# Optimization experiments

Measured on AMD Instinct MI355X. Metric: run time of the kernel, lower is better.

## Reference

```python
import jax, jax.numpy as jnp
import numpy as np
from collections import deque

SIGMA_LOW = 0.02  # TreeFilter2D(sigma=0.02); high-level trees use sigma=1 (low_tree=False)


def bilinear_resize(x, oh, ow):
    # torch F.interpolate(mode='bilinear', align_corners=False)
    B, C, H, W = x.shape
    sy, sx = H / oh, W / ow
    ys = jnp.maximum((jnp.arange(oh, dtype=jnp.float32) + 0.5) * sy - 0.5, 0.0)
    xs = jnp.maximum((jnp.arange(ow, dtype=jnp.float32) + 0.5) * sx - 0.5, 0.0)
    y0 = jnp.clip(jnp.floor(ys).astype(jnp.int32), 0, H - 1)
    x0 = jnp.clip(jnp.floor(xs).astype(jnp.int32), 0, W - 1)
    y1 = jnp.minimum(y0 + 1, H - 1)
    x1 = jnp.minimum(x0 + 1, W - 1)
    wy = (ys - y0).reshape(oh, 1)
    wx = (xs - x0).reshape(1, ow)
    top, bot = x[:, :, y0, :], x[:, :, y1, :]
    v00, v01 = top[:, :, :, x0], top[:, :, :, x1]
    v10, v11 = bot[:, :, :, x0], bot[:, :, :, x1]
    return ((1 - wy) * (1 - wx)) * v00 + ((1 - wy) * wx) * v01 + (wy * (1 - wx)) * v10 + (wy * wx) * v11


def nearest_resize(x, oh, ow):
    B, C, H, W = x.shape
    yi = jnp.minimum((jnp.arange(oh) * (H / oh)).astype(jnp.int32), H - 1)
    xi = jnp.minimum((jnp.arange(ow) * (W / ow)).astype(jnp.int32), W - 1)
    return x[:, :, yi, :][:, :, :, xi]


def _mst_adj(feat, h, w):
    # Kruskal MST on 4-connected grid; edge weight = norm2_distance of features.
    n = h * w
    idx = np.arange(n).reshape(h, w)
    eu = np.concatenate([idx[:, :-1].ravel(), idx[:-1, :].ravel()])
    ev = np.concatenate([idx[:, 1:].ravel(), idx[1:, :].ravel()])
    f = feat.reshape(feat.shape[0], -1).astype(np.float64)
    d = ((f[:, eu] - f[:, ev]) ** 2).sum(axis=0)
    order = np.argsort(d, kind='stable')
    pa = np.arange(n)

    def find(a):
        r = a
        while pa[r] != r:
            r = pa[r]
        while pa[a] != r:
            pa[a], a = r, pa[a]
        return r

    adj = [[] for _ in range(n)]
    cnt = 0
    for e in order:
        u, v = int(eu[e]), int(ev[e])
        ru, rv = find(u), find(v)
        if ru != rv:
            pa[ru] = rv
            adj[u].append(v)
            adj[v].append(u)
            cnt += 1
            if cnt == n - 1:
                break
    return adj


def build_forest(embed):
    # embed: np [B,C,h,w] -> global parent array (ids b*n+i) + per-BFS-level node lists
    B, C, h, w = embed.shape
    n = h * w
    parent = np.arange(B * n)
    level = np.zeros(B * n, dtype=np.int64)
    for b in range(B):
        adj = _mst_adj(embed[b], h, w)
        lv = np.full(n, -1, dtype=np.int64)
        lv[0] = 0
        q = deque([0])
        while q:
            u = q.popleft()
            for v in adj[u]:
                if lv[v] < 0:
                    lv[v] = lv[u] + 1
                    parent[b * n + v] = b * n + u
                    q.append(v)
        level[b * n:(b + 1) * n] = lv
    d = int(level.max())
    levels = [np.nonzero(level == l)[0] for l in range(1, d + 1)]
    return jnp.asarray(parent), levels


def tree_filter(feature, embed, parent, levels, sigma):
    # feature [B,C,n], embed [B,Ce,n]; normalized tree filtering:
    # y_i = sum_j prod(path-edge-weights) x_j / sum_j prod(path-edge-weights)
    B, C, n = feature.shape
    ones = jnp.ones((B, 1, n), feature.dtype)
    xg = jnp.moveaxis(jnp.concatenate([feature, ones], axis=1), 0, 1).reshape(C + 1, B * n)
    eg = jnp.moveaxis(embed, 0, 1).reshape(embed.shape[1], B * n)
    wgt = jnp.exp(-((eg - eg[:, parent]) ** 2).sum(axis=0) / sigma)  # [B*n]; root entries unused
    # upward (leaf->root) subtree aggregation
    A = xg
    for idx in reversed(levels):
        A = A.at[:, parent[idx]].add(wgt[idx] * A[:, idx])
    # downward (root->leaf) completion
    F = A
    for idx in levels:
        F = F.at[:, idx].set(A[:, idx] + wgt[idx] * (F[:, parent[idx]] - wgt[idx] * A[:, idx]))
    y = F[:C] / F[C]
    return jnp.moveaxis(y.reshape(C, B, n), 0, 1)  # [B,C,n]


def setup_inputs() -> dict:
    key = jax.random.key(0)
    ks = jax.random.split(key, 6)
    B, K, h, w = 8, 4, 48, 48
    C = 512
    preds = jax.random.normal(ks[0], (B, K, h, w), jnp.float32)
    low_feats = jax.random.uniform(ks[1], (B, 3, 192, 192), jnp.float32) * 0.1
    hf1 = jax.random.normal(ks[2], (B, C, 24, 24), jnp.float32) * 0.05
    hf2 = jax.random.normal(ks[3], (B, C, 12, 12), jnp.float32) * 0.05
    hf3 = jax.random.normal(ks[4], (B, C, 6, 6), jnp.float32) * 0.05
    rois = (jax.random.uniform(ks[5], (B, 192, 192)) > 0.5).astype(jnp.float32)
    weight = jnp.asarray(0.4, jnp.float32)
    return {"preds": preds, "low_feats": low_feats, "high_feats_1": hf1,
            "high_feats_2": hf2, "high_feats_3": hf3, "unlabeled_ROIs": rois,
            "weight": weight}


def reference(preds, low_feats, high_feats_1, high_feats_2, high_feats_3, unlabeled_ROIs, weight):
    B, K, h, w = preds.shape
    low = bilinear_resize(low_feats, h, w)                     # no_grad in original
    roi = nearest_resize(unlabeled_ROIs[:, None], h, w)        # [B,1,h,w]
    N = roi.sum()
    prob = jax.nn.softmax(preds, axis=1)
    probf = prob.reshape(B, K, -1)
    roif = roi.reshape(B, 1, -1)

    parent0, lv0 = build_forest(np.asarray(low))
    AS = tree_filter(probf, low.reshape(B, low.shape[1], -1), parent0, lv0, SIGMA_LOW)

    loss = jnp.zeros((), preds.dtype)
    for hf in (high_feats_1, high_feats_2, high_feats_3):
        hfi = bilinear_resize(hf, h, w)
        p, lv = build_forest(np.asarray(hfi))
        AS_k = tree_filter(AS, hfi.reshape(B, hfi.shape[1], -1), p, lv, 1.0)
        loss = loss + (roif * jnp.abs(probf - AS_k)).sum()
    loss = jnp.where(N > 0, loss / N, loss)
    return weight * loss
```

## Files before the change

### kernel.cpp

```cpp
#include <hip/hip_runtime.h>
#include <math.h>


#define HH 48
#define WW 48
#define NN (HH*WW)
#define EHH (HH*(WW-1))
#define EEE (2*EHH)
#define BB 8
#define KK 4
#define TPB 256
#define TPE 512
#define TPW 1024
#define TPF 512
#define NPL 5
#define NPN 5
#define LVE (2*(NN-1))
#define NIPT ((NN+TPW-1)/TPW)
#define SENTN 0xFFFFu
#define MAXT 12

__device__ __forceinline__ void edge_uv(int e,int& u,int& v){
  if(e<EHH){ int r=e/(WW-1); int c=e-r*(WW-1); u=r*WW+c; v=u+1; }
  else     { int t=e-EHH; u=t; v=t+WW; }
}

__device__ __forceinline__ void pick_src(int f, const float* lowf, const float* hf1,
                                         const float* hf2, const float* hf3,
                                         const float*& src, int& sh, int& C){
  if(f==0){src=lowf; sh=192; C=3;}
  else if(f==1){src=hf1; sh=24; C=512;}
  else if(f==2){src=hf2; sh=12; C=512;}
  else        {src=hf3; sh=6;  C=512;}
}

__global__ __launch_bounds__(TPE) void k_edges(
  const float* __restrict__ lowf, const float* __restrict__ hf1,
  const float* __restrict__ hf2, const float* __restrict__ hf3,
  const float* __restrict__ preds, float* __restrict__ probf,
  double* __restrict__ pd_low, double* __restrict__ pd_hf, int nchunk)
{
  __shared__ float up[4*NN+64];
  __shared__ int   y0t[48], y1t[48];
  __shared__ float wyt[48];
  const int tid=threadIdx.x;
  const int nEB=8+24*nchunk;

  if(blockIdx.x>=nEB){
    int t=(blockIdx.x-nEB)*TPE+tid;
    if(t<BB*NN){
      int b=t/NN, i=t-b*NN;
      const float* p=preds+(size_t)b*KK*NN+i;
      float x0=p[0],x1=p[NN],x2=p[2*NN],x3=p[3*NN];
      float mx=fmaxf(fmaxf(x0,x1),fmaxf(x2,x3));
      float e0=expf(x0-mx),e1=expf(x1-mx),e2=expf(x2-mx),e3=expf(x3-mx);
      float s=((e0+e1)+(e2+e3));
      float* q=probf+(size_t)b*KK*NN+i;
      q[0]=e0/s; q[NN]=e1/s; q[2*NN]=e2/s; q[3*NN]=e3/s;
    }
    return;
  }

  int pidx, chunk, hfidx=0;
  if(blockIdx.x<8){ pidx=blockIdx.x; chunk=0; }
  else { int t=blockIdx.x-8; hfidx=t/nchunk; chunk=t-hfidx*nchunk; pidx=8+hfidx; }
  const int f=pidx>>3, b=pidx&7;
  const float* src; int sh,C;
  pick_src(f,lowf,hf1,hf2,hf3,src,sh,C);
  const int shw=sh*sh;
  const float* srcb=src+(size_t)b*C*shw;
  const int cpc=(f==0)?3:(512/nchunk);
  const int c_begin=chunk*cpc;
  const int c_end=(c_begin+cpc<C)?(c_begin+cpc):C;

  if(tid<48){
    float sy=(float)sh/48.0f;
    float ys=fmaxf(((float)tid+0.5f)*sy-0.5f,0.0f);
    int y0=(int)ys; if(y0>sh-1) y0=sh-1;
    int y1=y0+1; if(y1>sh-1) y1=sh-1;
    y0t[tid]=y0; y1t[tid]=y1; wyt[tid]=ys-(float)y0;
  }

  double accH[NPN], accV[NPN];
  #pragma unroll
  for(int j=0;j<NPN;j++){ accH[j]=0.0; accV[j]=0.0; }

  for(int c0=c_begin;c0<c_end;c0+=4){
    const int nc=(c_end-c0<4)?(c_end-c0):4;
    __syncthreads();
    for(int i=tid;i<NN;i+=TPE){
      int r=i/WW, c=i-r*WW;
      int y0=y0t[r], y1=y1t[r]; float wy=wyt[r];
      int x0=y0t[c], x1=y1t[c]; float wx=wyt[c];
      float w00=(1.0f-wy)*(1.0f-wx), w01=(1.0f-wy)*wx;
      float w10=wy*(1.0f-wx),        w11=wy*wx;
      int o00=y0*sh+x0, o01=y0*sh+x1, o10=y1*sh+x0, o11=y1*sh+x1;
      const float* pl=srcb+(size_t)c0*shw;
      for(int cc=0;cc<nc;cc++){
        const float* p=pl+(size_t)cc*shw;
        up[cc*NN+i]=w00*p[o00]+w01*p[o01]+w10*p[o10]+w11*p[o11];
      }
    }
    __syncthreads();
    #pragma unroll
    for(int j=0;j<NPN;j++){
      int u=tid+j*TPE;
      if(u<NN){
        int r=u/WW, c=u-r*WW;
        bool hOK=(c<WW-1), vOK=(r<HH-1);
        for(int cc=0;cc<nc;cc++){
          const float* pu=up+cc*NN+u;
          float a=pu[0], b1=pu[1], c1=pu[WW];
          if(hOK){ double d=(double)a-(double)b1; accH[j]=fma(d,d,accH[j]); }
          if(vOK){ double d=(double)a-(double)c1; accV[j]=fma(d,d,accV[j]); }
        }
      }
    }
  }
  double* outp=(f==0)? pd_low+(size_t)pidx*EEE
                     : pd_hf+((size_t)hfidx*nchunk+chunk)*EEE;
  #pragma unroll
  for(int j=0;j<NPN;j++){
    int u=tid+j*TPE;
    if(u<NN){
      int r=u/WW, c=u-r*WW;
      if(c<WW-1) outp[r*(WW-1)+c]=accH[j];
      if(r<HH-1) outp[EHH+u]=accV[j];
    }
  }
}

__global__ __launch_bounds__(TPB) void k_redux(
  const double* __restrict__ pd_low, const double* __restrict__ pd_hf,
  int nchunk, double* __restrict__ dkeyG, int* __restrict__ cnt)
{
  int t=blockIdx.x*TPB+threadIdx.x;
  if(t==0) *cnt=0;
  if(t>=32*EEE) return;
  int pidx=t/EEE, e=t-pidx*EEE;
  double s;
  if(pidx<8) s=pd_low[(size_t)pidx*EEE+e];
  else {
    const double* p0=pd_hf+((size_t)(pidx-8)*nchunk)*EEE+e;
    s=0.0;
    for(int k=0;k<nchunk;k++) s+=p0[(size_t)k*EEE];
  }
  dkeyG[t]=s;
}

__global__ __launch_bounds__(TPW) void k_struct(
  const double* __restrict__ dkeyG, int* __restrict__ Tg,
  int2* __restrict__ apT)
{
  __shared__ __align__(16) char smem[123600];
  unsigned long long* keyE =(unsigned long long*)(smem+0);
  unsigned char*      mstf =(unsigned char*)(smem+36096);
  unsigned long long* best =(unsigned long long*)(smem+40608);
  int*                comp =(int*)(smem+59040);
  unsigned short*     uEdg =(unsigned short*)(smem+68256);
  int*                lnk  =(int*)(smem+77472);
  float4*             adjw =(float4*)(smem+40608);
  unsigned char*      adjS =(unsigned char*)(smem+77472);
  int*                chunkS=(int*)(smem+79776);
  unsigned int*       eA   =(unsigned int*)(smem+0);
  unsigned int*       eB   =(unsigned int*)(smem+18432);
  unsigned short*     uDE  =(unsigned short*)(smem+83872);
  int*                nodeoff=(int*)(smem+93088);
  int*                flags=(int*)(smem+123552);
  int*                ancA =(int*)(smem+0);
  float*              prmA =(float*)(smem+9216);
  int*                ancB =(int*)(smem+18432);
  float*              prmB =(float*)(smem+27648);

  const int tid=threadIdx.x;
  const int pidx=blockIdx.x;
  const int f=pidx>>3;
  const float sigma=(f==0)?0.02f:1.0f;
  const double* p0=dkeyG+(size_t)pidx*EEE;
  const int lane=tid&63, wid=tid>>6;
  int2* apT0=apT+(size_t)pidx*MAXT*NN;

  {
    for(int e=tid;e<EEE;e+=TPW){
      int u,v; edge_uv(e,u,v);
      uEdg[e]=(unsigned short)u;
      keyE[e]=(((unsigned long long)__double_as_longlong(p0[e]))&~0x1FFFull)
              |(unsigned long long)e;
      mstf[e]=0;
    }
    for(int i=tid;i<NN;i+=TPW){ comp[i]=i; best[i]=~0ull; lnk[i]=i; }
    if(tid==0) flags[1]=0;
    __syncthreads();

    for(int round=0;round<20;++round){
      for(int i=tid;i<NN;i+=TPW) lnk[i]=i;
      for(int e=tid;e<EEE;e+=TPW){
        int u=uEdg[e]; int v=(e<EHH)?u+1:u+WW;
        int cu=comp[u], cv=comp[v];
        if(cu!=cv){
          unsigned long long k=keyE[e];
          atomicMin(&best[cu],k);
          atomicMin(&best[cv],k);
        }
      }
      __syncthreads();
      for(int i=tid;i<NN;i+=TPW){
        if(comp[i]==i && best[i]!=~0ull){
          int e=(int)(best[i]&0x1FFFull);
          int u=uEdg[e]; int v=(e<EHH)?u+1:u+WW;
          int cu=comp[u], cv=comp[v];
          int other=(cu==i)?cv:cu;
          bool mutual=((best[other]&0x1FFFull)==(unsigned long long)e);
          if(!mutual || other<i){ lnk[i]=other; mstf[e]=1; flags[1]=1; }
        }
      }
      __syncthreads();
      if(flags[1]==0) break;
      {
        volatile int* vl=lnk;
        for(int i=tid;i<NN;i+=TPW){
          int x=comp[i];
          int p=vl[x];
          int gp=vl[p];
          while(p!=gp){
            vl[x]=gp;
            x=p; p=gp; gp=vl[p];
          }
          comp[i]=p;
        }
      }
      for(int i=tid;i<NN;i+=TPW) best[i]=~0ull;
      if(tid==0) flags[1]=0;
      __syncthreads();
    }
    __syncthreads();

    for(int i=tid;i<NN;i+=TPW){
      int r=i/WW, c=i-r*WW;
      int mask=0; float4 w; w.x=0.0f; w.y=0.0f; w.z=0.0f; w.w=0.0f;
      if(c>0    && mstf[r*(WW-1)+c-1]){ mask|=1; w.x=expf(-(float)p0[r*(WW-1)+c-1]/sigma); }
      if(c<WW-1 && mstf[r*(WW-1)+c])  { mask|=2; w.y=expf(-(float)p0[r*(WW-1)+c]/sigma); }
      if(r>0    && mstf[EHH+i-WW])    { mask|=4; w.z=expf(-(float)p0[EHH+i-WW]/sigma); }
      if(r<HH-1 && mstf[EHH+i])       { mask|=8; w.w=expf(-(float)p0[EHH+i]/sigma); }
      adjw[i]=w;
      adjS[i]=(unsigned char)mask;
    }
    __syncthreads();
  }

  {
    {
      const int base=tid*NIPT;
      int dg[NIPT], incl[NIPT]; int lsum=0;
      #pragma unroll
      for(int j=0;j<NIPT;j++){
        int i=base+j;
        dg[j]=(i<NN)?__popc((int)adjS[i]):0;
        lsum+=dg[j]; incl[j]=lsum;
      }
      int x=lsum;
      #pragma unroll
      for(int off=1;off<64;off<<=1){
        int y=__shfl_up(x,off,64);
        if(lane>=off) x+=y;
      }
      if(lane==63) chunkS[wid]=x;
      __syncthreads();
      if(wid==0 && lane<16){
        int w=chunkS[lane];
        #pragma unroll
        for(int off=1;off<16;off<<=1){
          int y=__shfl_up(w,off,64);
          if(lane>=off) w+=y;
        }
        chunkS[lane]=w;
      }
      __syncthreads();
      const int waveoff=(wid>0)?chunkS[wid-1]:0;
      const int myoff=x+waveoff-lsum;
      #pragma unroll
      for(int j=0;j<NIPT;j++){
        int i=base+j;
        if(i<NN) nodeoff[i]=myoff+incl[j]-dg[j];
      }
    }
    __syncthreads();

    for(int u=tid;u<NN;u+=TPW){
      int mu=adjS[u];
      int off=nodeoff[u];
      int m=mu;
      while(m){
        int d=__ffs(m)-1; m&=m-1;
        int ce=off+__popc(mu&((1<<d)-1));
        int v=(d==0)?u-1:(d==1)?u+1:(d==2)?u-WW:u+WW;
        int rd=d^1;
        int mv=adjS[v];
        int nd=rd;
        #pragma unroll
        for(int k2=4;k2>=1;k2--){ int dd=(rd+k2)&3; if(mv&(1<<dd)) nd=dd; }
        int ne=nodeoff[v]+__popc(mv&((1<<nd)-1));
        unsigned int nxt=(ne==0)?SENTN:(unsigned int)ne;
        uDE[ce]=(unsigned short)((u<<2)|d);
        eA[ce]=(nxt<<16)|1u;
      }
    }
    __syncthreads();

    unsigned int* P=eA; unsigned int* Q=eB;
    for(int r2=0;r2<13;r2++){
      for(int t=tid;t<LVE;t+=TPW){
        unsigned int pk=P[t];
        unsigned int dist=pk&0xFFFFu, nxt=pk>>16;
        if(nxt!=SENTN){
          unsigned int pk2=P[nxt];
          dist+=pk2&0xFFFFu;
          nxt=pk2>>16;
          pk=(nxt<<16)|dist;
        }
        Q[t]=pk;
      }
      __syncthreads();
      unsigned int* tmp=P; P=Q; Q=tmp;
    }

    if(tid==0) apT0[0]=make_int2(0,__float_as_int(0.0f));
    for(int t=tid;t<LVE;t+=TPW){
      int ud=uDE[t]; int u=ud>>2, d=ud&3;
      int v=(d==0)?u-1:(d==1)?u+1:(d==2)?u-WW:u+WW;
      int rce=nodeoff[v]+__popc(adjS[v]&((1<<(d^1))-1));
      unsigned int dist=P[t]&0xFFFFu, rdist=P[rce]&0xFFFFu;
      if(dist>rdist){
        float4 w4=adjw[u];
        float w=(d==0)?w4.x:(d==1)?w4.y:(d==2)?w4.z:w4.w;
        apT0[v]=make_int2(u,__float_as_int(w));
      }
    }
    __syncthreads();
  }

  {
    for(int t=tid;t<MAXT;t+=TPW) chunkS[t]=0;
    int* aP=ancA; int* aQ=ancB; float* pP=prmA; float* pQ=prmB;
    for(int i=tid;i<NN;i+=TPW){
      int2 rec=apT0[i];
      aP[i]=rec.x; pP[i]=__int_as_float(rec.y);
    }
    __syncthreads();
    int T=MAXT;
    for(int t=1;t<MAXT;t++){
      int any=0;
      for(int i=tid;i<NN;i+=TPW){
        int a=aP[i];
        int a2=aP[a]; float pr=pP[i]*pP[a];
        aQ[i]=a2; pQ[i]=pr;
        apT0[(size_t)t*NN+i]=make_int2(a2,__float_as_int(pr));
        if(pr!=0.0f) any=1;
      }
      if(any) chunkS[t]=1;
      __syncthreads();
      if(chunkS[t]==0){ T=t; break; }
      { int* t1=aP; aP=aQ; aQ=t1; float* t2=pP; pP=pQ; pQ=t2; }
    }
    if(tid==0) Tg[pidx]=T;
  }
}

__global__ __launch_bounds__(TPF) void k_fchan(
  const float* __restrict__ X, float* __restrict__ Fout,
  const int* __restrict__ Tg, const int2* __restrict__ apT,
  int pidx0, int dv)
{
  __shared__ float S[NN];
  __shared__ float Sb[NN];
  const int tid=threadIdx.x;
  const int pg=blockIdx.x/5, c=blockIdx.x%5;
  const int pidx=pidx0+pg;
  const int xb=pg&7;
  const int T=Tg[pidx];
  const int2* apP=apT+(size_t)pidx*MAXT*NN;

  float wv[NPL];
  #pragma unroll
  for(int j=0;j<NPL;j++){
    int i=tid+j*TPF;
    if(i<NN){
      int2 ap0=apP[i];
      wv[j]=__int_as_float(ap0.y);
      float val=1.0f;
      if(c<4){
        if(dv){
          float inv=1.0f/X[((size_t)xb*5+4)*NN+i];
          val=X[((size_t)xb*5+c)*NN+i]*inv;
        } else {
          val=X[((size_t)xb*KK+c)*NN+i];
        }
      }
      S[i]=val;
    } else wv[j]=0.0f;
  }
  __syncthreads();

  for(int t=0;t<T;t++){
    float sn[NPL]; int aj[NPL]; float pj[NPL];
    #pragma unroll
    for(int j=0;j<NPL;j++){
      int i=tid+j*TPF;
      if(i<NN){
        int2 ap=apP[(size_t)t*NN+i];
        sn[j]=S[i]; aj[j]=ap.x; pj[j]=__int_as_float(ap.y);
      }
      else { sn[j]=0.0f; aj[j]=0; pj[j]=0.0f; }
    }
    __syncthreads();
    #pragma unroll
    for(int j=0;j<NPL;j++){
      int i=tid+j*TPF;
      if(i<NN) atomicAdd(&S[aj[j]], pj[j]*sn[j]);
    }
    __syncthreads();
  }

  #pragma unroll
  for(int j=0;j<NPL;j++){
    int i=tid+j*TPF;
    if(i<NN){ float fq=1.0f-wv[j]*wv[j]; Sb[i]=fq*S[i]; }
  }
  __syncthreads();

  float* Sp=Sb; float* Sq=S;
  for(int t=0;t<T;t++){
    float bn[NPL];
    #pragma unroll
    for(int j=0;j<NPL;j++){
      int i=tid+j*TPF;
      if(i<NN){
        int2 ap=apP[(size_t)t*NN+i];
        bn[j]=fmaf(__int_as_float(ap.y),Sp[ap.x],Sp[i]);
      } else bn[j]=0.0f;
    }
    __syncthreads();
    #pragma unroll
    for(int j=0;j<NPL;j++){
      int i=tid+j*TPF;
      if(i<NN) Sq[i]=bn[j];
    }
    __syncthreads();
    { float* tmp=Sp; Sp=Sq; Sq=tmp; }
  }
  float* o=Fout+(size_t)blockIdx.x*NN;
  for(int i=tid;i<NN;i+=TPF) o[i]=Sp[i];
}

__global__ __launch_bounds__(TPB) void k_loss(
  const float* __restrict__ FB, const float* __restrict__ probf,
  const float* __restrict__ rois, float* __restrict__ partials,
  const float* __restrict__ wt, float* __restrict__ out, int* __restrict__ cnt)
{
  __shared__ float red[TPB];
  __shared__ int lastS;
  const int tid=threadIdx.x;
  const int fb=blockIdx.x;
  const int b=fb&7;
  const float* pb=probf+(size_t)b*KK*NN;
  float part=0.0f;
  for(int i=tid;i<NN;i+=TPB){
    int r=i/WW, c2=i-r*WW;
    float roi=rois[(size_t)b*(192*192)+(4*r)*192+(4*c2)];
    float inv=1.0f/FB[((size_t)fb*5+4)*NN+i];
    float s=fabsf(pb[i]      -FB[((size_t)fb*5+0)*NN+i]*inv)
          + fabsf(pb[NN+i]   -FB[((size_t)fb*5+1)*NN+i]*inv)
          + fabsf(pb[2*NN+i] -FB[((size_t)fb*5+2)*NN+i]*inv)
          + fabsf(pb[3*NN+i] -FB[((size_t)fb*5+3)*NN+i]*inv);
    part+=roi*s;
  }
  red[tid]=part; __syncthreads();
  for(int s2=TPB/2;s2>0;s2>>=1){ if(tid<s2) red[tid]+=red[tid+s2]; __syncthreads(); }
  if(tid==0){
    partials[fb]=red[0];
    __threadfence();
    int old=atomicAdd(cnt,1);
    lastS=(old==3*BB-1);
  }
  __syncthreads();
  if(!lastS) return;

  float n=0.0f;
  for(int t=tid;t<BB*NN;t+=TPB){
    int b2=t/NN, i=t-b2*NN; int r=i/WW, c=i-r*WW;
    n += rois[(size_t)b2*(192*192)+(4*r)*192+(4*c)];
  }
  red[tid]=n; __syncthreads();
  for(int s=TPB/2;s>0;s>>=1){ if(tid<s) red[tid]+=red[tid+s]; __syncthreads(); }
  if(tid==0){
    float loss=0.0f;
    for(int j=0;j<3*BB;j++) loss+=partials[j];
    float N=red[0];
    out[0]=wt[0]*((N>0.0f)?(loss/N):loss);
  }
}

extern "C" void kernel_launch(void* const* d_in, const int* in_sizes, int n_in,
                              void* d_out, int out_size, void* d_ws, size_t ws_size,
                              hipStream_t stream) {
  (void)in_sizes; (void)n_in; (void)out_size;
  const float* preds=(const float*)d_in[0];
  const float* lowf =(const float*)d_in[1];
  const float* hf1  =(const float*)d_in[2];
  const float* hf2  =(const float*)d_in[3];
  const float* hf3  =(const float*)d_in[4];
  const float* rois =(const float*)d_in[5];
  const float* wt   =(const float*)d_in[6];
  float* out=(float*)d_out;

  char* ws=(char*)d_ws;
  float* partials=(float*)ws;
  int*   cnt=(int*)(ws+128);
  float* probf=(float*)(ws+256);
  size_t tg_off=256+(size_t)2*BB*KK*NN*4;
  int*   Tg=(int*)(ws+tg_off);
  size_t dk_off=tg_off+256;
  double* dkeyG=(double*)(ws+dk_off);
  size_t pl_off=dk_off+(size_t)32*EEE*8;
  double* pd_low=(double*)(ws+pl_off);
  size_t ph_off=pl_off+(size_t)8*EEE*8;
  double* pd_hf=(double*)(ws+ph_off);

  int2*  apT=(int2*)(ws+ph_off);
  float* FA =(float*)(ws+ph_off+(size_t)32*MAXT*NN*8);
  float* FB =(float*)(ws+ph_off+(size_t)32*MAXT*NN*8+(size_t)40*NN*4);

  int nchunk=32;
  if(ph_off+(size_t)24*32*EEE*8>ws_size) nchunk=16;

  const int nEB=8+24*nchunk;
  const int nSM=(BB*NN+TPE-1)/TPE;
  k_edges<<<nEB+nSM,TPE,0,stream>>>(lowf,hf1,hf2,hf3,preds,probf,pd_low,pd_hf,nchunk);
  k_redux<<<(32*EEE+TPB-1)/TPB,TPB,0,stream>>>(pd_low,pd_hf,nchunk,dkeyG,cnt);
  k_struct<<<32,TPW,0,stream>>>(dkeyG,Tg,apT);
  k_fchan<<<40,TPF,0,stream>>>(probf,FA,Tg,apT,0,0);
  k_fchan<<<120,TPF,0,stream>>>(FA,FB,Tg,apT,8,1);
  k_loss<<<3*BB,TPB,0,stream>>>(FB,probf,rois,partials,wt,out,cnt);
}
```

Before: 210.5 us.

## Fuse structure, filter and loss kernels into one persistent kernel with global flags

Merges k_struct, both k_fchan passes and k_loss into a single 216-block launch. Blocks wait on each other through spin-waits on global atomic flags, so filter blocks for a given tree start as soon as that tree's structure is ready, with no kernel boundaries in between. The aim is to remove launch gaps and let stages overlap. In exchange, the filter and loss blocks now run with 1024 threads instead of 512 and 256. The scheme depends on all 216 blocks being co-resident, since otherwise the spin-waits could deadlock.

```diff
diff --git a/kernel.cpp b/kernel.cpp
--- a/kernel.cpp
+++ b/kernel.cpp
@@ -11,12 +11,11 @@
 #define KK 4
 #define TPB 256
 #define TPE 512
-#define TPW 1024
-#define TPF 512
-#define NPL 5
+#define TPM 1024
 #define NPN 5
+#define NPLM 3
 #define LVE (2*(NN-1))
-#define NIPT ((NN+TPW-1)/TPW)
+#define NIPT ((NN+TPM-1)/TPM)
 #define SENTN 0xFFFFu
 #define MAXT 12
 
@@ -132,10 +131,10 @@
 
 __global__ __launch_bounds__(TPB) void k_redux(
   const double* __restrict__ pd_low, const double* __restrict__ pd_hf,
-  int nchunk, double* __restrict__ dkeyG, int* __restrict__ cnt)
+  int nchunk, double* __restrict__ dkeyG, int* __restrict__ flagsG)
 {
   int t=blockIdx.x*TPB+threadIdx.x;
-  if(t==0) *cnt=0;
+  if(t<65) flagsG[t]=0;
   if(t>=32*EEE) return;
   int pidx=t/EEE, e=t-pidx*EEE;
   double s;
@@ -148,53 +147,59 @@
   dkeyG[t]=s;
 }
 
-__global__ __launch_bounds__(TPW) void k_struct(
+__global__ __launch_bounds__(TPM) void k_mega(
   const double* __restrict__ dkeyG, int* __restrict__ Tg,
-  int2* __restrict__ apT)
+  int2* __restrict__ apT, const float* __restrict__ probf,
+  float* __restrict__ FA, float* __restrict__ FB,
+  const float* __restrict__ rois, float* __restrict__ partials,
+  const float* __restrict__ wt, float* __restrict__ out,
+  int* __restrict__ flagsG)
 {
-  __shared__ __align__(16) char smem[123600];
-  unsigned long long* keyE =(unsigned long long*)(smem+0);
-  unsigned char*      mstf =(unsigned char*)(smem+36096);
-  unsigned long long* best =(unsigned long long*)(smem+40608);
-  int*                comp =(int*)(smem+59040);
-  unsigned short*     uEdg =(unsigned short*)(smem+68256);
-  int*                lnk  =(int*)(smem+77472);
-  float4*             adjw =(float4*)(smem+40608);
-  unsigned char*      adjS =(unsigned char*)(smem+77472);
-  int*                chunkS=(int*)(smem+79776);
-  unsigned int*       eA   =(unsigned int*)(smem+0);
-  unsigned int*       eB   =(unsigned int*)(smem+18432);
-  unsigned short*     uDE  =(unsigned short*)(smem+83872);
-  int*                nodeoff=(int*)(smem+93088);
-  int*                flags=(int*)(smem+123552);
-  int*                ancA =(int*)(smem+0);
-  float*              prmA =(float*)(smem+9216);
-  int*                ancB =(int*)(smem+18432);
-  float*              prmB =(float*)(smem+27648);
-
+  __shared__ __align__(16) char smem[123904];
   const int tid=threadIdx.x;
-  const int pidx=blockIdx.x;
-  const int f=pidx>>3;
-  const float sigma=(f==0)?0.02f:1.0f;
-  const double* p0=dkeyG+(size_t)pidx*EEE;
-  const int lane=tid&63, wid=tid>>6;
-  int2* apT0=apT+(size_t)pidx*MAXT*NN;
-
-  {
-    for(int e=tid;e<EEE;e+=TPW){
+  const int bid=blockIdx.x;
+
+  if(bid<32){
+    unsigned long long* keyE =(unsigned long long*)(smem+0);
+    unsigned char*      mstf =(unsigned char*)(smem+36096);
+    unsigned long long* best =(unsigned long long*)(smem+40608);
+    int*                comp =(int*)(smem+59040);
+    unsigned short*     uEdg =(unsigned short*)(smem+68256);
+    int*                lnk  =(int*)(smem+77472);
+    float4*             adjw =(float4*)(smem+40608);
+    unsigned char*      adjS =(unsigned char*)(smem+77472);
+    int*                chunkS=(int*)(smem+79776);
+    unsigned int*       eA   =(unsigned int*)(smem+0);
+    unsigned int*       eB   =(unsigned int*)(smem+18432);
+    unsigned short*     uDE  =(unsigned short*)(smem+83872);
+    int*                nodeoff=(int*)(smem+93088);
+    int*                flags=(int*)(smem+123552);
+    int*                ancA =(int*)(smem+0);
+    float*              prmA =(float*)(smem+9216);
+    int*                ancB =(int*)(smem+18432);
+    float*              prmB =(float*)(smem+27648);
+
+    const int pidx=bid;
+    const int f=pidx>>3;
+    const float sigma=(f==0)?0.02f:1.0f;
+    const double* p0=dkeyG+(size_t)pidx*EEE;
+    const int lane=tid&63, wid=tid>>6;
+    int2* apT0=apT+(size_t)pidx*MAXT*NN;
+
+    for(int e=tid;e<EEE;e+=TPM){
       int u,v; edge_uv(e,u,v);
       uEdg[e]=(unsigned short)u;
       keyE[e]=(((unsigned long long)__double_as_longlong(p0[e]))&~0x1FFFull)
               |(unsigned long long)e;
       mstf[e]=0;
     }
-    for(int i=tid;i<NN;i+=TPW){ comp[i]=i; best[i]=~0ull; lnk[i]=i; }
+    for(int i=tid;i<NN;i+=TPM){ comp[i]=i; best[i]=~0ull; lnk[i]=i; }
     if(tid==0) flags[1]=0;
     __syncthreads();
 
     for(int round=0;round<20;++round){
-      for(int i=tid;i<NN;i+=TPW) lnk[i]=i;
-      for(int e=tid;e<EEE;e+=TPW){
+      for(int i=tid;i<NN;i+=TPM) lnk[i]=i;
+      for(int e=tid;e<EEE;e+=TPM){
         int u=uEdg[e]; int v=(e<EHH)?u+1:u+WW;
         int cu=comp[u], cv=comp[v];
         if(cu!=cv){
@@ -204,7 +209,7 @@
         }
       }
       __syncthreads();
-      for(int i=tid;i<NN;i+=TPW){
+      for(int i=tid;i<NN;i+=TPM){
         if(comp[i]==i && best[i]!=~0ull){
           int e=(int)(best[i]&0x1FFFull);
           int u=uEdg[e]; int v=(e<EHH)?u+1:u+WW;
@@ -218,7 +223,7 @@
       if(flags[1]==0) break;
       {
         volatile int* vl=lnk;
-        for(int i=tid;i<NN;i+=TPW){
+        for(int i=tid;i<NN;i+=TPM){
           int x=comp[i];
           int p=vl[x];
           int gp=vl[p];
@@ -229,13 +234,13 @@
           comp[i]=p;
         }
       }
-      for(int i=tid;i<NN;i+=TPW) best[i]=~0ull;
+      for(int i=tid;i<NN;i+=TPM) best[i]=~0ull;
       if(tid==0) flags[1]=0;
       __syncthreads();
     }
     __syncthreads();
 
-    for(int i=tid;i<NN;i+=TPW){
+    for(int i=tid;i<NN;i+=TPM){
       int r=i/WW, c=i-r*WW;
       int mask=0; float4 w; w.x=0.0f; w.y=0.0f; w.z=0.0f; w.w=0.0f;
       if(c>0    && mstf[r*(WW-1)+c-1]){ mask|=1; w.x=expf(-(float)p0[r*(WW-1)+c-1]/sigma); }
@@ -246,9 +251,7 @@
       adjS[i]=(unsigned char)mask;
     }
     __syncthreads();
-  }
-
-  {
+
     {
       const int base=tid*NIPT;
       int dg[NIPT], incl[NIPT]; int lsum=0;
@@ -286,7 +289,7 @@
     }
     __syncthreads();
 
-    for(int u=tid;u<NN;u+=TPW){
+    for(int u=tid;u<NN;u+=TPM){
       int mu=adjS[u];
       int off=nodeoff[u];
       int m=mu;
@@ -309,7 +312,7 @@
 
     unsigned int* P=eA; unsigned int* Q=eB;
     for(int r2=0;r2<13;r2++){
-      for(int t=tid;t<LVE;t+=TPW){
+      for(int t=tid;t<LVE;t+=TPM){
         unsigned int pk=P[t];
         unsigned int dist=pk&0xFFFFu, nxt=pk>>16;
         if(nxt!=SENTN){
@@ -325,7 +328,7 @@
     }
 
     if(tid==0) apT0[0]=make_int2(0,__float_as_int(0.0f));
-    for(int t=tid;t<LVE;t+=TPW){
+    for(int t=tid;t<LVE;t+=TPM){
       int ud=uDE[t]; int u=ud>>2, d=ud&3;
       int v=(d==0)?u-1:(d==1)?u+1:(d==2)?u-WW:u+WW;
       int rce=nodeoff[v]+__popc(adjS[v]&((1<<(d^1))-1));
@@ -337,166 +340,176 @@
       }
     }
     __syncthreads();
+
+    {
+      for(int t=tid;t<MAXT;t+=TPM) chunkS[t]=0;
+      int* aP=ancA; int* aQ=ancB; float* pP=prmA; float* pQ=prmB;
+      for(int i=tid;i<NN;i+=TPM){
+        int2 rec=apT0[i];
+        aP[i]=rec.x; pP[i]=__int_as_float(rec.y);
+      }
+      __syncthreads();
+      int T=MAXT;
+      for(int t=1;t<MAXT;t++){
+        int any=0;
+        for(int i=tid;i<NN;i+=TPM){
+          int a=aP[i];
+          int a2=aP[a]; float pr=pP[i]*pP[a];
+          aQ[i]=a2; pQ[i]=pr;
+          apT0[(size_t)t*NN+i]=make_int2(a2,__float_as_int(pr));
+          if(pr!=0.0f) any=1;
+        }
+        if(any) chunkS[t]=1;
+        __syncthreads();
+        if(chunkS[t]==0){ T=t; break; }
+        { int* t1=aP; aP=aQ; aQ=t1; float* t2=pP; pP=pQ; pQ=t2; }
+      }
+      if(tid==0) Tg[pidx]=T;
+    }
+    __syncthreads();
+    if(tid==0){ __threadfence(); atomicExch(&flagsG[1+pidx],1); }
+    return;
+  }
+
+  if(bid<192){
+    float* S =(float*)smem;
+    float* Sb=(float*)(smem+9216);
+    int pidx, xb, c, dv; float* o;
+    if(bid<72){ int k=bid-32; int pg=k/5; c=k%5; pidx=pg; xb=pg; dv=0;
+                o=FA+(size_t)k*NN; }
+    else      { int k=bid-72; int pg=k/5; c=k%5; pidx=8+pg; xb=pg&7; dv=1;
+                o=FB+(size_t)k*NN; }
+    if(tid==0){
+      while(atomicAdd(&flagsG[1+pidx],0)==0){}
+      if(dv) while(atomicAdd(&flagsG[33+xb],0)<5){}
+    }
+    __syncthreads();
+    __threadfence();
+    const int T=Tg[pidx];
+    const int2* apP=apT+(size_t)pidx*MAXT*NN;
+    const float* X=dv? FA : probf;
+
+    float wv[NPLM];
+    #pragma unroll
+    for(int j=0;j<NPLM;j++){
+      int i=tid+j*TPM;
+      if(i<NN){
+        int2 ap0=apP[i];
+        wv[j]=__int_as_float(ap0.y);
+        float val=1.0f;
+        if(c<4){
+          if(dv){
+            float inv=1.0f/X[((size_t)xb*5+4)*NN+i];
+            val=X[((size_t)xb*5+c)*NN+i]*inv;
+          } else {
+            val=X[((size_t)xb*KK+c)*NN+i];
+          }
+        }
+        S[i]=val;
+      } else wv[j]=0.0f;
+    }
+    __syncthreads();
+
+    for(int t=0;t<T;t++){
+      float sn[NPLM]; int aj[NPLM]; float pj[NPLM];
+      #pragma unroll
+      for(int j=0;j<NPLM;j++){
+        int i=tid+j*TPM;
+        if(i<NN){
+          int2 ap=apP[(size_t)t*NN+i];
+          sn[j]=S[i]; aj[j]=ap.x; pj[j]=__int_as_float(ap.y);
+        } else { sn[j]=0.0f; aj[j]=0; pj[j]=0.0f; }
+      }
+      __syncthreads();
+      #pragma unroll
+      for(int j=0;j<NPLM;j++){
+        int i=tid+j*TPM;
+        if(i<NN) atomicAdd(&S[aj[j]], pj[j]*sn[j]);
+      }
+      __syncthreads();
+    }
+
+    #pragma unroll
+    for(int j=0;j<NPLM;j++){
+      int i=tid+j*TPM;
+      if(i<NN){ float fq=1.0f-wv[j]*wv[j]; Sb[i]=fq*S[i]; }
+    }
+    __syncthreads();
+
+    float* Sp=Sb; float* Sq=S;
+    for(int t=0;t<T;t++){
+      float bn[NPLM];
+      #pragma unroll
+      for(int j=0;j<NPLM;j++){
+        int i=tid+j*TPM;
+        if(i<NN){
+          int2 ap=apP[(size_t)t*NN+i];
+          bn[j]=fmaf(__int_as_float(ap.y),Sp[ap.x],Sp[i]);
+        } else bn[j]=0.0f;
+      }
+      __syncthreads();
+      #pragma unroll
+      for(int j=0;j<NPLM;j++){
+        int i=tid+j*TPM;
+        if(i<NN) Sq[i]=bn[j];
+      }
+      __syncthreads();
+      { float* tmp=Sp; Sp=Sq; Sq=tmp; }
+    }
+    for(int i=tid;i<NN;i+=TPM) o[i]=Sp[i];
+    __syncthreads();
+    if(tid==0){
+      __threadfence();
+      if(dv) atomicAdd(&flagsG[41+(bid-72)/5],1);
+      else   atomicAdd(&flagsG[33+(bid-32)/5],1);
+    }
+    return;
   }
 
   {
-    for(int t=tid;t<MAXT;t+=TPW) chunkS[t]=0;
-    int* aP=ancA; int* aQ=ancB; float* pP=prmA; float* pQ=prmB;
-    for(int i=tid;i<NN;i+=TPW){
-      int2 rec=apT0[i];
-      aP[i]=rec.x; pP[i]=__int_as_float(rec.y);
-    }
-    __syncthreads();
-    int T=MAXT;
-    for(int t=1;t<MAXT;t++){
-      int any=0;
-      for(int i=tid;i<NN;i+=TPW){
-        int a=aP[i];
-        int a2=aP[a]; float pr=pP[i]*pP[a];
-        aQ[i]=a2; pQ[i]=pr;
-        apT0[(size_t)t*NN+i]=make_int2(a2,__float_as_int(pr));
-        if(pr!=0.0f) any=1;
-      }
-      if(any) chunkS[t]=1;
-      __syncthreads();
-      if(chunkS[t]==0){ T=t; break; }
-      { int* t1=aP; aP=aQ; aQ=t1; float* t2=pP; pP=pQ; pQ=t2; }
-    }
-    if(tid==0) Tg[pidx]=T;
-  }
-}
-
-__global__ __launch_bounds__(TPF) void k_fchan(
-  const float* __restrict__ X, float* __restrict__ Fout,
-  const int* __restrict__ Tg, const int2* __restrict__ apT,
-  int pidx0, int dv)
-{
-  __shared__ float S[NN];
-  __shared__ float Sb[NN];
-  const int tid=threadIdx.x;
-  const int pg=blockIdx.x/5, c=blockIdx.x%5;
-  const int pidx=pidx0+pg;
-  const int xb=pg&7;
-  const int T=Tg[pidx];
-  const int2* apP=apT+(size_t)pidx*MAXT*NN;
-
-  float wv[NPL];
-  #pragma unroll
-  for(int j=0;j<NPL;j++){
-    int i=tid+j*TPF;
-    if(i<NN){
-      int2 ap0=apP[i];
-      wv[j]=__int_as_float(ap0.y);
-      float val=1.0f;
-      if(c<4){
-        if(dv){
-          float inv=1.0f/X[((size_t)xb*5+4)*NN+i];
-          val=X[((size_t)xb*5+c)*NN+i]*inv;
-        } else {
-          val=X[((size_t)xb*KK+c)*NN+i];
-        }
-      }
-      S[i]=val;
-    } else wv[j]=0.0f;
-  }
-  __syncthreads();
-
-  for(int t=0;t<T;t++){
-    float sn[NPL]; int aj[NPL]; float pj[NPL];
-    #pragma unroll
-    for(int j=0;j<NPL;j++){
-      int i=tid+j*TPF;
-      if(i<NN){
-        int2 ap=apP[(size_t)t*NN+i];
-        sn[j]=S[i]; aj[j]=ap.x; pj[j]=__int_as_float(ap.y);
-      }
-      else { sn[j]=0.0f; aj[j]=0; pj[j]=0.0f; }
-    }
-    __syncthreads();
-    #pragma unroll
-    for(int j=0;j<NPL;j++){
-      int i=tid+j*TPF;
-      if(i<NN) atomicAdd(&S[aj[j]], pj[j]*sn[j]);
-    }
-    __syncthreads();
-  }
-
-  #pragma unroll
-  for(int j=0;j<NPL;j++){
-    int i=tid+j*TPF;
-    if(i<NN){ float fq=1.0f-wv[j]*wv[j]; Sb[i]=fq*S[i]; }
-  }
-  __syncthreads();
-
-  float* Sp=Sb; float* Sq=S;
-  for(int t=0;t<T;t++){
-    float bn[NPL];
-    #pragma unroll
-    for(int j=0;j<NPL;j++){
-      int i=tid+j*TPF;
-      if(i<NN){
-        int2 ap=apP[(size_t)t*NN+i];
-        bn[j]=fmaf(__int_as_float(ap.y),Sp[ap.x],Sp[i]);
-      } else bn[j]=0.0f;
-    }
-    __syncthreads();
-    #pragma unroll
-    for(int j=0;j<NPL;j++){
-      int i=tid+j*TPF;
-      if(i<NN) Sq[i]=bn[j];
-    }
-    __syncthreads();
-    { float* tmp=Sp; Sp=Sq; Sq=tmp; }
-  }
-  float* o=Fout+(size_t)blockIdx.x*NN;
-  for(int i=tid;i<NN;i+=TPF) o[i]=Sp[i];
-}
-
-__global__ __launch_bounds__(TPB) void k_loss(
-  const float* __restrict__ FB, const float* __restrict__ probf,
-  const float* __restrict__ rois, float* __restrict__ partials,
-  const float* __restrict__ wt, float* __restrict__ out, int* __restrict__ cnt)
-{
-  __shared__ float red[TPB];
-  __shared__ int lastS;
-  const int tid=threadIdx.x;
-  const int fb=blockIdx.x;
-  const int b=fb&7;
-  const float* pb=probf+(size_t)b*KK*NN;
-  float part=0.0f;
-  for(int i=tid;i<NN;i+=TPB){
-    int r=i/WW, c2=i-r*WW;
-    float roi=rois[(size_t)b*(192*192)+(4*r)*192+(4*c2)];
-    float inv=1.0f/FB[((size_t)fb*5+4)*NN+i];
-    float s=fabsf(pb[i]      -FB[((size_t)fb*5+0)*NN+i]*inv)
-          + fabsf(pb[NN+i]   -FB[((size_t)fb*5+1)*NN+i]*inv)
-          + fabsf(pb[2*NN+i] -FB[((size_t)fb*5+2)*NN+i]*inv)
-          + fabsf(pb[3*NN+i] -FB[((size_t)fb*5+3)*NN+i]*inv);
-    part+=roi*s;
-  }
-  red[tid]=part; __syncthreads();
-  for(int s2=TPB/2;s2>0;s2>>=1){ if(tid<s2) red[tid]+=red[tid+s2]; __syncthreads(); }
-  if(tid==0){
-    partials[fb]=red[0];
+    float* red=(float*)smem;
+    __shared__ int lastS;
+    const int fb=bid-192;
+    const int b=fb&7;
+    if(tid==0){ while(atomicAdd(&flagsG[41+fb],0)<5){} }
+    __syncthreads();
     __threadfence();
-    int old=atomicAdd(cnt,1);
-    lastS=(old==3*BB-1);
-  }
-  __syncthreads();
-  if(!lastS) return;
-
-  float n=0.0f;
-  for(int t=tid;t<BB*NN;t+=TPB){
-    int b2=t/NN, i=t-b2*NN; int r=i/WW, c=i-r*WW;
-    n += rois[(size_t)b2*(192*192)+(4*r)*192+(4*c)];
-  }
-  red[tid]=n; __syncthreads();
-  for(int s=TPB/2;s>0;s>>=1){ if(tid<s) red[tid]+=red[tid+s]; __syncthreads(); }
-  if(tid==0){
-    float loss=0.0f;
-    for(int j=0;j<3*BB;j++) loss+=partials[j];
-    float N=red[0];
-    out[0]=wt[0]*((N>0.0f)?(loss/N):loss);
+    const float* pb=probf+(size_t)b*KK*NN;
+    float part=0.0f;
+    for(int i=tid;i<NN;i+=TPM){
+      int r=i/WW, c2=i-r*WW;
+      float roi=rois[(size_t)b*(192*192)+(4*r)*192+(4*c2)];
+      float inv=1.0f/FB[((size_t)fb*5+4)*NN+i];
+      float s=fabsf(pb[i]      -FB[((size_t)fb*5+0)*NN+i]*inv)
+            + fabsf(pb[NN+i]   -FB[((size_t)fb*5+1)*NN+i]*inv)
+            + fabsf(pb[2*NN+i] -FB[((size_t)fb*5+2)*NN+i]*inv)
+            + fabsf(pb[3*NN+i] -FB[((size_t)fb*5+3)*NN+i]*inv);
+      part+=roi*s;
+    }
+    red[tid]=part; __syncthreads();
+    for(int s2=TPM/2;s2>0;s2>>=1){ if(tid<s2) red[tid]+=red[tid+s2]; __syncthreads(); }
+    if(tid==0){
+      partials[fb]=red[0];
+      __threadfence();
+      int old=atomicAdd(&flagsG[0],1);
+      lastS=(old==3*BB-1);
+    }
+    __syncthreads();
+    if(!lastS) return;
+
+    float n=0.0f;
+    for(int t=tid;t<BB*NN;t+=TPM){
+      int b2=t/NN, i=t-b2*NN; int r=i/WW, c=i-r*WW;
+      n += rois[(size_t)b2*(192*192)+(4*r)*192+(4*c)];
+    }
+    red[tid]=n; __syncthreads();
+    for(int s=TPM/2;s>0;s>>=1){ if(tid<s) red[tid]+=red[tid+s]; __syncthreads(); }
+    if(tid==0){
+      float loss=0.0f;
+      for(int j=0;j<3*BB;j++) loss+=partials[j];
+      float N=red[0];
+      out[0]=wt[0]*((N>0.0f)?(loss/N):loss);
+    }
   }
 }
 
@@ -514,10 +527,10 @@
   float* out=(float*)d_out;
 
   char* ws=(char*)d_ws;
-  float* partials=(float*)ws;
-  int*   cnt=(int*)(ws+128);
-  float* probf=(float*)(ws+256);
-  size_t tg_off=256+(size_t)2*BB*KK*NN*4;
+  int*   flagsG=(int*)ws;
+  float* partials=(float*)(ws+512);
+  float* probf=(float*)(ws+768);
+  size_t tg_off=768+(size_t)BB*KK*NN*4;
   int*   Tg=(int*)(ws+tg_off);
   size_t dk_off=tg_off+256;
   double* dkeyG=(double*)(ws+dk_off);
@@ -536,9 +549,6 @@
   const int nEB=8+24*nchunk;
   const int nSM=(BB*NN+TPE-1)/TPE;
   k_edges<<<nEB+nSM,TPE,0,stream>>>(lowf,hf1,hf2,hf3,preds,probf,pd_low,pd_hf,nchunk);
-  k_redux<<<(32*EEE+TPB-1)/TPB,TPB,0,stream>>>(pd_low,pd_hf,nchunk,dkeyG,cnt);
-  k_struct<<<32,TPW,0,stream>>>(dkeyG,Tg,apT);
-  k_fchan<<<40,TPF,0,stream>>>(probf,FA,Tg,apT,0,0);
-  k_fchan<<<120,TPF,0,stream>>>(FA,FB,Tg,apT,8,1);
-  k_loss<<<3*BB,TPB,0,stream>>>(FB,probf,rois,partials,wt,out,cnt);
+  k_redux<<<(32*EEE+TPB-1)/TPB,TPB,0,stream>>>(pd_low,pd_hf,nchunk,dkeyG,flagsG);
+  k_mega<<<216,TPM,0,stream>>>(dkeyG,Tg,apT,probf,FA,FB,rois,partials,wt,out,flagsG);
 }
```

After: 235.8 us. +12.0%, slower.
